# Kernel optimization log

Hardware: AMD Instinct MI355X
Metric: run time of the kernel (lower is better)

## Reference

```python
import jax, jax.numpy as jnp
import numpy as np

B, L = 16384, 50
SIMPLE_BUCKETS = [100000] * 6
SHARE_BUCKET = 1000000
NAMES = [f"f{i}" for i in range(6)] + ["s0", "s1"]
BUCKETS = SIMPLE_BUCKETS + [SHARE_BUCKET, SHARE_BUCKET]
PAD_FRAC = 0.3  # fraction of -1 padding per row


def setup_inputs() -> dict:
    key = jax.random.key(0)
    inp = {}
    for i, (n, b) in enumerate(zip(NAMES, BUCKETS)):
        kv, kp = jax.random.split(jax.random.fold_in(key, i))
        vals = jax.random.randint(kv, (B, L), 0, 1_000_000_000, dtype=jnp.int32)
        pad = jax.random.uniform(kp, (B, L)) < PAD_FRAC
        inp[n] = jnp.where(pad, jnp.int32(-1), vals)
    for i, (n, b) in enumerate(zip(NAMES, BUCKETS)):
        kw = jax.random.fold_in(key, 100 + i)
        inp["W_" + n] = jax.random.normal(kw, (b,), dtype=jnp.float32) * 0.01
    inp["bias"] = jnp.zeros((1,), dtype=jnp.float32)
    return inp


def _feature_contrib(x, W, bucket):
    """Hashed multi-hot encode + sparse linear combine for one feature.

    x: [B, L] int32, padded with -1.  W: [bucket] float.
    Equivalent to (multihot(x) @ W) where multihot has a 1 at each distinct
    hashed bin present in the row (binary CategoryEncoding), but without
    materializing the [B, bucket] one-hot tensor.
    """
    valid = x >= 0
    bins = jnp.where(valid, x % bucket, bucket)  # sentinel `bucket` for padding
    s = jnp.sort(bins, axis=1)                   # [B, L] sorted bins per row
    first = jnp.concatenate(
        [jnp.ones_like(s[:, :1], dtype=bool), s[:, 1:] != s[:, :-1]], axis=1)
    mask = first & (s < bucket)                  # count each bin once, skip pad
    w = W[jnp.clip(s, 0, bucket - 1)]            # [B, L] gather
    return jnp.sum(jnp.where(mask, w, 0.0), axis=1)  # [B]


def reference(f0, f1, f2, f3, f4, f5, s0, s1,
              W_f0, W_f1, W_f2, W_f3, W_f4, W_f5, W_s0, W_s1, bias):
    feats = [f0, f1, f2, f3, f4, f5, s0, s1]
    weights = [W_f0, W_f1, W_f2, W_f3, W_f4, W_f5, W_s0, W_s1]
    out = bias[0]
    for x, W, b in zip(feats, weights, BUCKETS):
        out = out + _feature_contrib(x, W, b)
    return out[:, None]  # [B, 1], LinearModel with units=1
```

## Files before the change

### kernel.cpp

```cpp
#include <hip/hip_runtime.h>


constexpr int B = 16384;
constexpr int L = 50;
constexpr int SLOTS = 128;

struct KArgs {
    const int*   x[8];
    const float* w[8];
    const float* bias;
    float*       out;
};

__global__ __launch_bounds__(256) void wide_winner_kernel(KArgs a) {
    __shared__ unsigned tbl[4][SLOTS];

    const int wave = threadIdx.x >> 6;
    const int lane = threadIdx.x & 63;
    const int row  = (blockIdx.x << 2) | wave;

    int v[8];
    #pragma unroll
    for (int f = 0; f < 8; ++f)
        v[f] = (lane < L) ? a.x[f][row * L + lane] : -1;

    volatile unsigned* t = tbl[wave];

    float acc = 0.0f;

    #pragma unroll
    for (int f = 0; f < 8; ++f) {
        const bool valid = (v[f] >= 0);
        const unsigned bin = (f < 6) ? ((unsigned)v[f] % 100000u)
                                     : ((unsigned)v[f] % 1000000u);

        t[lane]      = 0xFFFFFFFFu;
        t[lane + 64] = 0xFFFFFFFFu;

        const unsigned packed = (bin << 6) | (unsigned)lane;
        unsigned h = (bin * 2654435761u) >> 25;
        bool pend = valid, keep = false;

        while (__any(pend)) {
            if (pend) {
                t[h] = packed;
                const unsigned r = t[h];
                if ((r >> 6) == bin) {
                    keep = (r == packed);
                    pend = false;
                } else {
                    h = (h + 1) & (SLOTS - 1);
                }
            }
        }

        if (keep) acc += a.w[f][bin];
    }

    #pragma unroll
    for (int off = 32; off; off >>= 1)
        acc += __shfl_xor(acc, off, 64);

    if (lane == 0) a.out[row] = acc + a.bias[0];
}

extern "C" void kernel_launch(void* const* d_in, const int* in_sizes, int n_in,
                              void* d_out, int out_size, void* d_ws, size_t ws_size,
                              hipStream_t stream) {
    KArgs a;
    for (int i = 0; i < 8; ++i) a.x[i] = (const int*)d_in[i];
    for (int i = 0; i < 8; ++i) a.w[i] = (const float*)d_in[8 + i];
    a.bias = (const float*)d_in[16];
    a.out  = (float*)d_out;

    wide_winner_kernel<<<B / 4, 256, 0, stream>>>(a);
}
```

Before: 39.32 us.

## Split work per feature across XCDs, convert shared weights to fp16, atomically accumulate

Blocks now cover one (feature, 4-row) pair instead of four rows across all eight features. blockIdx & 7 selects the feature, so consecutive blocks, which are likely placed round-robin across the eight XCDs, each keep one weight table hot in their own L2. The two 1M-entry shared tables are converted to fp16 in a pre-pass kernel each call to shrink the gather footprint. The output is initialized with bias and filled by atomicAdd. This adds two extra launches, a 2M-element conversion pass per call, fp16 rounding error on two features, and atomic contention.

```diff
diff --git a/kernel.cpp b/kernel.cpp
--- a/kernel.cpp
+++ b/kernel.cpp
@@ -1,77 +1,103 @@
 #include <hip/hip_runtime.h>
+#include <hip/hip_fp16.h>
 
 
 constexpr int B = 16384;
 constexpr int L = 50;
 constexpr int SLOTS = 128;
+constexpr int SSZ = 1000000;
 
 struct KArgs {
-    const int*   x[8];
-    const float* w[8];
-    const float* bias;
-    float*       out;
+    const int*    x[8];
+    const float*  wf[6];
+    const __half* ws0;
+    const __half* ws1;
+    float*        out;
 };
 
-__global__ __launch_bounds__(256) void wide_winner_kernel(KArgs a) {
+__global__ __launch_bounds__(256) void conv_s_kernel(const float* __restrict__ s0,
+                                                     const float* __restrict__ s1,
+                                                     __half* __restrict__ dst) {
+    const int e = (blockIdx.x * 256 + (int)threadIdx.x) * 4;
+    if (e >= 2 * SSZ) return;
+    const float* src = (e < SSZ) ? s0 : s1;
+    const int idx    = (e < SSZ) ? e  : e - SSZ;
+    const float4 v = reinterpret_cast<const float4*>(src)[idx >> 2];
+    *reinterpret_cast<__half2*>(dst + e)     = __floats2half2_rn(v.x, v.y);
+    *reinterpret_cast<__half2*>(dst + e + 2) = __floats2half2_rn(v.z, v.w);
+}
+
+__global__ __launch_bounds__(256) void init_kernel(float* out, const float* bias) {
+    const int i = blockIdx.x * 256 + (int)threadIdx.x;
+    out[i] = bias[0];
+}
+
+__global__ __launch_bounds__(256) void wide_xcd_kernel(KArgs a) {
     __shared__ unsigned tbl[4][SLOTS];
 
     const int wave = threadIdx.x >> 6;
     const int lane = threadIdx.x & 63;
-    const int row  = (blockIdx.x << 2) | wave;
+    const int feat = (int)(blockIdx.x & 7u);
+    const int row  = (int)((blockIdx.x >> 3) * 4) + wave;
 
-    int v[8];
-    #pragma unroll
-    for (int f = 0; f < 8; ++f)
-        v[f] = (lane < L) ? a.x[f][row * L + lane] : -1;
+    int v = -1;
+    if (lane < L) v = __builtin_nontemporal_load(a.x[feat] + row * L + lane);
+    const bool valid = (v >= 0);
+
+    const unsigned bin = (feat < 6) ? ((unsigned)v % 100000u)
+                                    : ((unsigned)v % 1000000u);
 
     volatile unsigned* t = tbl[wave];
+    t[lane]      = 0xFFFFFFFFu;
+    t[lane + 64] = 0xFFFFFFFFu;
+
+    const unsigned packed = (bin << 6) | (unsigned)lane;
+    unsigned h = (bin * 2654435761u) >> 25;
+    bool pend = valid, keep = false;
+
+    while (__any(pend)) {
+        if (pend) {
+            t[h] = packed;
+            const unsigned r = t[h];
+            if ((r >> 6) == bin) {
+                keep = (r == packed);
+                pend = false;
+            } else {
+                h = (h + 1) & (SLOTS - 1);
+            }
+        }
+    }
 
     float acc = 0.0f;
-
-    #pragma unroll
-    for (int f = 0; f < 8; ++f) {
-        const bool valid = (v[f] >= 0);
-        const unsigned bin = (f < 6) ? ((unsigned)v[f] % 100000u)
-                                     : ((unsigned)v[f] % 1000000u);
-
-        t[lane]      = 0xFFFFFFFFu;
-        t[lane + 64] = 0xFFFFFFFFu;
-
-        const unsigned packed = (bin << 6) | (unsigned)lane;
-        unsigned h = (bin * 2654435761u) >> 25;
-        bool pend = valid, keep = false;
-
-        while (__any(pend)) {
-            if (pend) {
-                t[h] = packed;
-                const unsigned r = t[h];
-                if ((r >> 6) == bin) {
-                    keep = (r == packed);
-                    pend = false;
-                } else {
-                    h = (h + 1) & (SLOTS - 1);
-                }
-            }
-        }
-
-        if (keep) acc += a.w[f][bin];
+    if (keep) {
+        if (feat < 6) acc = a.wf[feat][bin];
+        else          acc = __half2float((feat == 6 ? a.ws0 : a.ws1)[bin]);
     }
 
     #pragma unroll
     for (int off = 32; off; off >>= 1)
         acc += __shfl_xor(acc, off, 64);
 
-    if (lane == 0) a.out[row] = acc + a.bias[0];
+    if (lane == 0) atomicAdd(&a.out[row], acc);
 }
 
 extern "C" void kernel_launch(void* const* d_in, const int* in_sizes, int n_in,
                               void* d_out, int out_size, void* d_ws, size_t ws_size,
                               hipStream_t stream) {
+    __half* wbase = (__half*)d_ws;
+
+    conv_s_kernel<<<(2 * SSZ / 4 + 255) / 256, 256, 0, stream>>>(
+        (const float*)d_in[14], (const float*)d_in[15], wbase);
+
+    init_kernel<<<B / 256, 256, 0, stream>>>((float*)d_out,
+                                             (const float*)d_in[16]);
+
     KArgs a;
-    for (int i = 0; i < 8; ++i) a.x[i] = (const int*)d_in[i];
-    for (int i = 0; i < 8; ++i) a.w[i] = (const float*)d_in[8 + i];
-    a.bias = (const float*)d_in[16];
-    a.out  = (float*)d_out;
+    for (int i = 0; i < 8; ++i) a.x[i]  = (const int*)d_in[i];
+    for (int i = 0; i < 6; ++i) a.wf[i] = (const float*)d_in[8 + i];
+    a.ws0 = wbase;
+    a.ws1 = wbase + SSZ;
+    a.out = (float*)d_out;
 
-    wide_winner_kernel<<<B / 4, 256, 0, stream>>>(a);
+    wide_xcd_kernel<<<8 * (B / 4), 256, 0, stream>>>(a);
 }
```

After: 54.35 us. 38.2% more time.
